# Kernel optimization log

Hardware: AMD Instinct MI355X
Metric: run time of the kernel (lower is better)

Reference implementation:

```python
import jax, jax.numpy as jnp
import numpy as np

SPACIAL_SCALE = 1.0 / 32
POOLED = 7  # original uses (pooled_height, pooled_height) for both dims


def setup_inputs() -> dict:
    key = jax.random.key(0)
    k_f, k_b, k_x, k_y = jax.random.split(key, 4)
    N, C, H, W = 4, 256, 64, 64
    R = 256
    img = 2047.0  # image-space extent (stride 32 -> 64 feature cells)
    features = jax.random.normal(k_f, (N, C, H, W), dtype=jnp.float32)
    bidx = jax.random.randint(k_b, (R,), 0, N).astype(jnp.float32)
    xs = jnp.sort(jax.random.uniform(k_x, (R, 2), dtype=jnp.float32) * img, axis=1)
    ys = jnp.sort(jax.random.uniform(k_y, (R, 2), dtype=jnp.float32) * img, axis=1)
    # roi = (batch_idx, x_min, y_min, x_max, y_max)
    rois = jnp.stack([bidx, xs[:, 0], ys[:, 0], xs[:, 1], ys[:, 1]], axis=1)
    return {"features": features, "rois": rois}


def _roi_pool(features, rois):
    N, C, H, W = features.shape
    P = POOLED
    neg = -jnp.inf

    bidx = rois[:, 0].astype(jnp.int32)
    # np.round rounds half-to-even; jnp.round matches
    bbox = jnp.round(rois[:, 1:] * SPACIAL_SCALE).astype(jnp.int32)  # [R,4]
    x0 = jnp.clip(bbox[:, 0], 0, W - 1)
    y0 = jnp.clip(bbox[:, 1], 0, H - 1)
    x1 = jnp.clip(bbox[:, 2], 0, W - 1)
    y1 = jnp.clip(bbox[:, 3], 0, H - 1)
    valid = (x0 < x1) & (y0 < y1)  # [R]

    g = features[bidx]  # [R,C,H,W] gathered per-roi feature maps
    Lh = x1 - x0  # rows (H axis) get the x-range -- quirk of the original slice
    Lw = y1 - y0  # cols (W axis) get the y-range

    idx_h = jnp.arange(H)
    idx_w = jnp.arange(W)

    # adaptive_max_pool2d bins: start=floor(i*L/P), end=ceil((i+1)*L/P)
    # Stage 1: reduce W axis into P column bins -> [R,C,H,P]
    cols = []
    for j in range(P):
        s = y0 + (j * Lw) // P
        e = y0 + ((j + 1) * Lw + P - 1) // P
        m = (idx_w[None, :] >= s[:, None]) & (idx_w[None, :] < e[:, None])  # [R,W]
        cols.append(jnp.max(jnp.where(m[:, None, None, :], g, neg), axis=-1))
    s1 = jnp.stack(cols, axis=-1)  # [R,C,H,P]

    # Stage 2: reduce H axis into P row bins -> [R,C,P,P]
    rows = []
    for i in range(P):
        s = x0 + (i * Lh) // P
        e = x0 + ((i + 1) * Lh + P - 1) // P
        m = (idx_h[None, :] >= s[:, None]) & (idx_h[None, :] < e[:, None])  # [R,H]
        rows.append(jnp.max(jnp.where(m[:, None, :, None], s1, neg), axis=2))
    out = jnp.stack(rows, axis=2)  # [R,C,P,P]

    # degenerate rois stay zero (pooled initialized with torch.zeros)
    return jnp.where(valid[:, None, None, None], out, jnp.zeros((), out.dtype))


def reference(features, rois):
    return _roi_pool(features, rois)
```

## Files before the change

kernel.cpp:

```cpp
#include <hip/hip_runtime.h>
#include <math.h>

#define P 7
#define PP (P * P)
#define C 256
#define H 64
#define W 64
#define S (H * W)
#define R_MAX 1024

#define TS 32
__global__ __launch_bounds__(256) void transpose_kernel(
    const float* __restrict__ in, float* __restrict__ outT)
{
    __shared__ float tile[TS][TS + 1];
    const int b  = blockIdx.z;
    const int s0 = blockIdx.x * TS;
    const int c0 = blockIdx.y * TS;
    const int tx = threadIdx.x;
    const int ty = threadIdx.y;

    const float* ip = in + ((size_t)b * C + c0) * S + s0;
    #pragma unroll
    for (int k = 0; k < 4; ++k)
        tile[ty + 8 * k][tx] = ip[(size_t)(ty + 8 * k) * S + tx];

    __syncthreads();

    float* op = outT + ((size_t)b * S + s0) * C + c0;
    #pragma unroll
    for (int k = 0; k < 4; ++k)
        op[(size_t)(ty + 8 * k) * C + tx] = tile[tx][ty + 8 * k];
}

__global__ __launch_bounds__(256) void bucket_kernel(
    const float* __restrict__ rois, int* __restrict__ perm, int R)
{
    __shared__ int bimg[R_MAX];
    for (int t = threadIdx.x; t < R; t += blockDim.x)
        bimg[t] = (int)rois[(size_t)t * 5];
    __syncthreads();
    for (int t = threadIdx.x; t < R; t += blockDim.x) {
        const int myb = bimg[t];
        int pos = 0;
        for (int k = 0; k < R; ++k) {
            const int bk = bimg[k];
            pos += (bk < myb) || (bk == myb && k < t);
        }
        perm[pos] = t;
    }
}

__global__ __launch_bounds__(64) void roi_pool_cell_kernel(
    const float* __restrict__ ft,
    const float* __restrict__ rois,
    const int*   __restrict__ perm,
    float* __restrict__ ws2)
{
    const int l   = blockIdx.x;
    const int nwg = gridDim.x;
    const int work = ((nwg & 7) == 0) ? ((l & 7) * (nwg >> 3) + (l >> 3)) : l;

    const int rslot = work / PP;
    const int cell  = work % PP;
    const int i     = cell / P;
    const int j     = cell % P;
    const int c4    = threadIdx.x;

    const int r = perm[rslot];

    const float* roi = rois + (size_t)r * 5;
    const int b = (int)roi[0];
    int x0 = (int)rintf(roi[1] * 0.03125f);
    int y0 = (int)rintf(roi[2] * 0.03125f);
    int x1 = (int)rintf(roi[3] * 0.03125f);
    int y1 = (int)rintf(roi[4] * 0.03125f);
    x0 = min(max(x0, 0), W - 1);
    y0 = min(max(y0, 0), H - 1);
    x1 = min(max(x1, 0), W - 1);
    y1 = min(max(y1, 0), H - 1);

    float4* o = (float4*)(ws2 + ((size_t)rslot * PP + cell) * C) + c4;

    if (!((x0 < x1) && (y0 < y1))) {
        *o = make_float4(0.0f, 0.0f, 0.0f, 0.0f);
        return;
    }

    const int Lh = x1 - x0;
    const int Lw = y1 - y0;

    const int hs = x0 + (i * Lh) / P;
    const int he = x0 + ((i + 1) * Lh + (P - 1)) / P;
    const int ws = y0 + (j * Lw) / P;
    const int we = y0 + ((j + 1) * Lw + (P - 1)) / P;

    const int bh = he - hs;
    const int bw = we - ws;

    const float* base = ft + (((size_t)b * H + hs) * W + ws) * C + c4 * 4;

    float mx = -INFINITY, my = -INFINITY, mz = -INFINITY, mw = -INFINITY;

    for (int h = 0; h < bh; h += 2) {
        const int h2 = min(h + 1, bh - 1);
        const float* r0 = base + (size_t)h  * (W * C);
        const float* r1 = base + (size_t)h2 * (W * C);
        for (int w = 0; w < bw; w += 2) {
            const int w2 = min(w + 1, bw - 1);
            const float4 a  = *(const float4*)(r0 + (size_t)w  * C);
            const float4 bb = *(const float4*)(r0 + (size_t)w2 * C);
            const float4 cc = *(const float4*)(r1 + (size_t)w  * C);
            const float4 dd = *(const float4*)(r1 + (size_t)w2 * C);
            mx = fmaxf(fmaxf(fmaxf(mx, a.x), fmaxf(bb.x, cc.x)), dd.x);
            my = fmaxf(fmaxf(fmaxf(my, a.y), fmaxf(bb.y, cc.y)), dd.y);
            mz = fmaxf(fmaxf(fmaxf(mz, a.z), fmaxf(bb.z, cc.z)), dd.z);
            mw = fmaxf(fmaxf(fmaxf(mw, a.w), fmaxf(bb.w, cc.w)), dd.w);
        }
    }

    *o = make_float4(mx, my, mz, mw);
}

#define LPAD 257
__global__ __launch_bounds__(256) void reorder_kernel(
    const float* __restrict__ ws2,
    const int*   __restrict__ perm,
    float* __restrict__ out)
{
    __shared__ float lds[PP * LPAD];
    const int l = blockIdx.x;
    const int R = gridDim.x;
    const int rslot = ((R & 7) == 0) ? ((l & 7) * (R >> 3) + (l >> 3)) : l;
    const int r = perm[rslot];
    const int tid = threadIdx.x;

    const float* src = ws2 + (size_t)rslot * PP * C;
    #pragma unroll
    for (int cell = 0; cell < PP; ++cell)
        lds[cell * LPAD + tid] = src[(size_t)cell * C + tid];

    __syncthreads();

    float* dst = out + (size_t)r * C * PP;
    const int nq = (C * PP) / 4;
    #pragma unroll
    for (int k = 0; k < 13; ++k) {
        const int q = tid + 256 * k;
        if (q < nq) {
            float v[4];
            #pragma unroll
            for (int m = 0; m < 4; ++m) {
                const int idx  = 4 * q + m;
                const int c    = idx / PP;
                const int cell = idx % PP;
                v[m] = lds[cell * LPAD + c];
            }
            *(float4*)(dst + 4 * q) = make_float4(v[0], v[1], v[2], v[3]);
        }
    }
}

__global__ __launch_bounds__(64) void roi_pool_cell_direct_kernel(
    const float* __restrict__ ft, const float* __restrict__ rois,
    float* __restrict__ out)
{
    const int bid = blockIdx.x;
    const int r   = bid / PP;
    const int rem = bid % PP;
    const int i   = rem / P;
    const int j   = rem % P;
    const int c4  = threadIdx.x;

    const float* roi = rois + (size_t)r * 5;
    const int b = (int)roi[0];
    int x0 = (int)rintf(roi[1] * 0.03125f);
    int y0 = (int)rintf(roi[2] * 0.03125f);
    int x1 = (int)rintf(roi[3] * 0.03125f);
    int y1 = (int)rintf(roi[4] * 0.03125f);
    x0 = min(max(x0, 0), W - 1);
    y0 = min(max(y0, 0), H - 1);
    x1 = min(max(x1, 0), W - 1);
    y1 = min(max(y1, 0), H - 1);

    float* o = out + (((size_t)r * C + c4 * 4) * P + i) * P + j;
    if (!((x0 < x1) && (y0 < y1))) {
        o[0] = 0.0f; o[PP] = 0.0f; o[2 * PP] = 0.0f; o[3 * PP] = 0.0f;
        return;
    }
    const int Lh = x1 - x0, Lw = y1 - y0;
    const int hs = x0 + (i * Lh) / P;
    const int he = x0 + ((i + 1) * Lh + (P - 1)) / P;
    const int ws = y0 + (j * Lw) / P;
    const int we = y0 + ((j + 1) * Lw + (P - 1)) / P;
    const int bh = he - hs, bw = we - ws;
    const float* base = ft + (((size_t)b * H + hs) * W + ws) * C + c4 * 4;
    float mx = -INFINITY, my = -INFINITY, mz = -INFINITY, mw = -INFINITY;
    for (int h = 0; h < bh; h += 2) {
        const int h2 = min(h + 1, bh - 1);
        const float* r0 = base + (size_t)h  * (W * C);
        const float* r1 = base + (size_t)h2 * (W * C);
        for (int w = 0; w < bw; w += 2) {
            const int w2 = min(w + 1, bw - 1);
            const float4 a  = *(const float4*)(r0 + (size_t)w  * C);
            const float4 bb = *(const float4*)(r0 + (size_t)w2 * C);
            const float4 cc = *(const float4*)(r1 + (size_t)w  * C);
            const float4 dd = *(const float4*)(r1 + (size_t)w2 * C);
            mx = fmaxf(fmaxf(fmaxf(mx, a.x), fmaxf(bb.x, cc.x)), dd.x);
            my = fmaxf(fmaxf(fmaxf(my, a.y), fmaxf(bb.y, cc.y)), dd.y);
            mz = fmaxf(fmaxf(fmaxf(mz, a.z), fmaxf(bb.z, cc.z)), dd.z);
            mw = fmaxf(fmaxf(fmaxf(mw, a.w), fmaxf(bb.w, cc.w)), dd.w);
        }
    }
    o[0] = mx; o[PP] = my; o[2 * PP] = mz; o[3 * PP] = mw;
}

__global__ __launch_bounds__(256) void roi_pool_naive_kernel(
    const float* __restrict__ features, const float* __restrict__ rois,
    float* __restrict__ out)
{
    const int rb = blockIdx.x;
    const int r = rb / P;
    const int i = rb % P;
    const int c = threadIdx.x;

    const float* roi = rois + (size_t)r * 5;
    const int b = (int)roi[0];
    int x0 = (int)rintf(roi[1] * 0.03125f);
    int y0 = (int)rintf(roi[2] * 0.03125f);
    int x1 = (int)rintf(roi[3] * 0.03125f);
    int y1 = (int)rintf(roi[4] * 0.03125f);
    x0 = min(max(x0, 0), W - 1);
    y0 = min(max(y0, 0), H - 1);
    x1 = min(max(x1, 0), W - 1);
    y1 = min(max(y1, 0), H - 1);

    const bool valid = (x0 < x1) && (y0 < y1);
    float* o = out + (((size_t)r * C + c) * P + i) * P;
    if (!valid) {
        #pragma unroll
        for (int j = 0; j < P; ++j) o[j] = 0.0f;
        return;
    }
    const int Lh = x1 - x0, Lw = y1 - y0;
    const int hs = x0 + (i * Lh) / P;
    const int he = x0 + ((i + 1) * Lh + (P - 1)) / P;
    int ws_[P], we_[P];
    #pragma unroll
    for (int j = 0; j < P; ++j) {
        ws_[j] = y0 + (j * Lw) / P;
        we_[j] = y0 + ((j + 1) * Lw + (P - 1)) / P;
    }
    float acc[P];
    #pragma unroll
    for (int j = 0; j < P; ++j) acc[j] = -INFINITY;
    const float* f = features + (((size_t)b * C + c) * H) * W;
    for (int h = hs; h < he; ++h) {
        const float* row = f + h * W;
        #pragma unroll
        for (int j = 0; j < P; ++j) {
            float m = acc[j];
            for (int w = ws_[j]; w < we_[j]; ++w) m = fmaxf(m, row[w]);
            acc[j] = m;
        }
    }
    #pragma unroll
    for (int j = 0; j < P; ++j) o[j] = acc[j];
}

extern "C" void kernel_launch(void* const* d_in, const int* in_sizes, int n_in,
                              void* d_out, int out_size, void* d_ws, size_t ws_size,
                              hipStream_t stream)
{
    const float* features = (const float*)d_in[0];
    const float* rois     = (const float*)d_in[1];
    float* out = (float*)d_out;

    const int R = in_sizes[1] / 5;
    const int N = in_sizes[0] / (C * S);

    const size_t ft_bytes  = (size_t)N * C * S * sizeof(float);
    const size_t ws2_bytes = (size_t)R * PP * C * sizeof(float);
    const size_t perm_bytes = (size_t)R * sizeof(int);
    const size_t full_need = ft_bytes + ws2_bytes + perm_bytes;

    if (ws_size >= full_need && R <= R_MAX) {
        float* ft  = (float*)d_ws;
        float* ws2 = (float*)((char*)d_ws + ft_bytes);
        int*  perm = (int*)((char*)d_ws + ft_bytes + ws2_bytes);

        dim3 tgrid(S / TS, C / TS, N);
        transpose_kernel<<<tgrid, dim3(TS, 8), 0, stream>>>(features, ft);
        bucket_kernel<<<1, 256, 0, stream>>>(rois, perm, R);
        roi_pool_cell_kernel<<<R * PP, 64, 0, stream>>>(ft, rois, perm, ws2);
        reorder_kernel<<<R, 256, 0, stream>>>(ws2, perm, out);
    } else if (ws_size >= ft_bytes) {
        float* ft = (float*)d_ws;
        dim3 tgrid(S / TS, C / TS, N);
        transpose_kernel<<<tgrid, dim3(TS, 8), 0, stream>>>(features, ft);
        roi_pool_cell_direct_kernel<<<R * PP, 64, 0, stream>>>(ft, rois, out);
    } else {
        roi_pool_naive_kernel<<<R * P, C, 0, stream>>>(features, rois, out);
    }
}
```

Measured before the change: 41.85 us.

## Fuse ROI pooling and output reorder into one kernel per channel group

Replaces the per-cell pooling kernel and separate reorder kernel with a single kernel where each 64-thread block handles one ROI and a 32-channel group across all 49 cells. Results are staged in shared memory and written directly in [C,P,P] order, which removes the intermediate workspace round trip and one kernel launch. Per-thread work grows to up to 7 cells with serial loops, and the work-swizzle now assumes the grid is a multiple of 8 unconditionally.

```diff
diff --git a/kernel.cpp b/kernel.cpp
--- a/kernel.cpp
+++ b/kernel.cpp
@@ -8,6 +8,11 @@
 #define W 64
 #define S (H * W)
 #define R_MAX 1024
+
+#define CH 32
+#define NCG (C / CH)
+#define ITEMS (PP * (CH / 4))
+#define LDS_PAD (PP + 1)
 
 #define TS 32
 __global__ __launch_bounds__(256) void transpose_kernel(
@@ -51,24 +56,23 @@
     }
 }
 
-__global__ __launch_bounds__(64) void roi_pool_cell_kernel(
+__global__ __launch_bounds__(64) void roi_pool_fused_kernel(
     const float* __restrict__ ft,
     const float* __restrict__ rois,
     const int*   __restrict__ perm,
-    float* __restrict__ ws2)
-{
+    float* __restrict__ out)
+{
+    __shared__ float lds[CH * LDS_PAD];
+
     const int l   = blockIdx.x;
     const int nwg = gridDim.x;
-    const int work = ((nwg & 7) == 0) ? ((l & 7) * (nwg >> 3) + (l >> 3)) : l;
-
-    const int rslot = work / PP;
-    const int cell  = work % PP;
-    const int i     = cell / P;
-    const int j     = cell % P;
-    const int c4    = threadIdx.x;
+    const int work  = (l & 7) * (nwg >> 3) + (l >> 3);
+    const int rslot = work / NCG;
+    const int cg    = work % NCG;
+    const int t     = threadIdx.x;
+    const int cbase = cg * CH;
 
     const int r = perm[rslot];
-
     const float* roi = rois + (size_t)r * 5;
     const int b = (int)roi[0];
     int x0 = (int)rintf(roi[1] * 0.03125f);
@@ -80,83 +84,84 @@
     x1 = min(max(x1, 0), W - 1);
     y1 = min(max(y1, 0), H - 1);
 
-    float4* o = (float4*)(ws2 + ((size_t)rslot * PP + cell) * C) + c4;
-
-    if (!((x0 < x1) && (y0 < y1))) {
-        *o = make_float4(0.0f, 0.0f, 0.0f, 0.0f);
-        return;
-    }
-
-    const int Lh = x1 - x0;
-    const int Lw = y1 - y0;
-
-    const int hs = x0 + (i * Lh) / P;
-    const int he = x0 + ((i + 1) * Lh + (P - 1)) / P;
-    const int ws = y0 + (j * Lw) / P;
-    const int we = y0 + ((j + 1) * Lw + (P - 1)) / P;
-
-    const int bh = he - hs;
-    const int bw = we - ws;
-
-    const float* base = ft + (((size_t)b * H + hs) * W + ws) * C + c4 * 4;
-
-    float mx = -INFINITY, my = -INFINITY, mz = -INFINITY, mw = -INFINITY;
-
-    for (int h = 0; h < bh; h += 2) {
-        const int h2 = min(h + 1, bh - 1);
-        const float* r0 = base + (size_t)h  * (W * C);
-        const float* r1 = base + (size_t)h2 * (W * C);
-        for (int w = 0; w < bw; w += 2) {
-            const int w2 = min(w + 1, bw - 1);
-            const float4 a  = *(const float4*)(r0 + (size_t)w  * C);
-            const float4 bb = *(const float4*)(r0 + (size_t)w2 * C);
-            const float4 cc = *(const float4*)(r1 + (size_t)w  * C);
-            const float4 dd = *(const float4*)(r1 + (size_t)w2 * C);
-            mx = fmaxf(fmaxf(fmaxf(mx, a.x), fmaxf(bb.x, cc.x)), dd.x);
-            my = fmaxf(fmaxf(fmaxf(my, a.y), fmaxf(bb.y, cc.y)), dd.y);
-            mz = fmaxf(fmaxf(fmaxf(mz, a.z), fmaxf(bb.z, cc.z)), dd.z);
-            mw = fmaxf(fmaxf(fmaxf(mw, a.w), fmaxf(bb.w, cc.w)), dd.w);
-        }
-    }
-
-    *o = make_float4(mx, my, mz, mw);
-}
-
-#define LPAD 257
-__global__ __launch_bounds__(256) void reorder_kernel(
-    const float* __restrict__ ws2,
-    const int*   __restrict__ perm,
-    float* __restrict__ out)
-{
-    __shared__ float lds[PP * LPAD];
-    const int l = blockIdx.x;
-    const int R = gridDim.x;
-    const int rslot = ((R & 7) == 0) ? ((l & 7) * (R >> 3) + (l >> 3)) : l;
-    const int r = perm[rslot];
-    const int tid = threadIdx.x;
-
-    const float* src = ws2 + (size_t)rslot * PP * C;
-    #pragma unroll
-    for (int cell = 0; cell < PP; ++cell)
-        lds[cell * LPAD + tid] = src[(size_t)cell * C + tid];
+    const bool valid = (x0 < x1) && (y0 < y1);
+
+    if (valid) {
+        const int Lh = x1 - x0;
+        const int Lw = y1 - y0;
+        #pragma unroll
+        for (int k = 0; k < 7; ++k) {
+            const int item = t + 64 * k;
+            if (item < ITEMS) {
+                const int cell = item >> 3;
+                const int q    = item & 7;
+                const int i    = cell / P;
+                const int j    = cell - P * i;
+
+                const int hs = x0 + (i * Lh) / P;
+                const int he = x0 + ((i + 1) * Lh + (P - 1)) / P;
+                const int ws = y0 + (j * Lw) / P;
+                const int we = y0 + ((j + 1) * Lw + (P - 1)) / P;
+                const int bh = he - hs;
+                const int bw = we - ws;
+
+                const float* base = ft + (((size_t)b * H + hs) * W + ws) * C + cbase + q * 4;
+
+                float mx = -INFINITY, my = -INFINITY, mz = -INFINITY, mw = -INFINITY;
+                for (int h = 0; h < bh; h += 2) {
+                    const int h2 = min(h + 1, bh - 1);
+                    const float* r0 = base + (size_t)h  * (W * C);
+                    const float* r1 = base + (size_t)h2 * (W * C);
+                    for (int w = 0; w < bw; w += 2) {
+                        const int w2 = min(w + 1, bw - 1);
+                        const float4 a  = *(const float4*)(r0 + (size_t)w  * C);
+                        const float4 bb = *(const float4*)(r0 + (size_t)w2 * C);
+                        const float4 cc = *(const float4*)(r1 + (size_t)w  * C);
+                        const float4 dd = *(const float4*)(r1 + (size_t)w2 * C);
+                        mx = fmaxf(fmaxf(fmaxf(mx, a.x), fmaxf(bb.x, cc.x)), dd.x);
+                        my = fmaxf(fmaxf(fmaxf(my, a.y), fmaxf(bb.y, cc.y)), dd.y);
+                        mz = fmaxf(fmaxf(fmaxf(mz, a.z), fmaxf(bb.z, cc.z)), dd.z);
+                        mw = fmaxf(fmaxf(fmaxf(mw, a.w), fmaxf(bb.w, cc.w)), dd.w);
+                    }
+                }
+                const int cl = q * 4;
+                lds[(cl + 0) * LDS_PAD + cell] = mx;
+                lds[(cl + 1) * LDS_PAD + cell] = my;
+                lds[(cl + 2) * LDS_PAD + cell] = mz;
+                lds[(cl + 3) * LDS_PAD + cell] = mw;
+            }
+        }
+    } else {
+        #pragma unroll
+        for (int k = 0; k < 7; ++k) {
+            const int item = t + 64 * k;
+            if (item < ITEMS) {
+                const int cell = item >> 3;
+                const int cl   = (item & 7) * 4;
+                lds[(cl + 0) * LDS_PAD + cell] = 0.0f;
+                lds[(cl + 1) * LDS_PAD + cell] = 0.0f;
+                lds[(cl + 2) * LDS_PAD + cell] = 0.0f;
+                lds[(cl + 3) * LDS_PAD + cell] = 0.0f;
+            }
+        }
+    }
 
     __syncthreads();
 
-    float* dst = out + (size_t)r * C * PP;
-    const int nq = (C * PP) / 4;
-    #pragma unroll
-    for (int k = 0; k < 13; ++k) {
-        const int q = tid + 256 * k;
-        if (q < nq) {
+    float* dst = out + ((size_t)r * C + cbase) * PP;
+    #pragma unroll
+    for (int k = 0; k < 7; ++k) {
+        const int fq = t + 64 * k;
+        if (fq < ITEMS) {
             float v[4];
             #pragma unroll
             for (int m = 0; m < 4; ++m) {
-                const int idx  = 4 * q + m;
-                const int c    = idx / PP;
-                const int cell = idx % PP;
-                v[m] = lds[cell * LPAD + c];
+                const int idx  = 4 * fq + m;
+                const int cl   = idx / PP;
+                const int cell = idx - PP * cl;
+                v[m] = lds[cl * LDS_PAD + cell];
             }
-            *(float4*)(dst + 4 * q) = make_float4(v[0], v[1], v[2], v[3]);
+            *(float4*)(dst + 4 * fq) = make_float4(v[0], v[1], v[2], v[3]);
         }
     }
 }
@@ -279,21 +284,18 @@
     const int R = in_sizes[1] / 5;
     const int N = in_sizes[0] / (C * S);
 
-    const size_t ft_bytes  = (size_t)N * C * S * sizeof(float);
-    const size_t ws2_bytes = (size_t)R * PP * C * sizeof(float);
+    const size_t ft_bytes   = (size_t)N * C * S * sizeof(float);
     const size_t perm_bytes = (size_t)R * sizeof(int);
-    const size_t full_need = ft_bytes + ws2_bytes + perm_bytes;
+    const size_t full_need  = ft_bytes + perm_bytes;
 
     if (ws_size >= full_need && R <= R_MAX) {
         float* ft  = (float*)d_ws;
-        float* ws2 = (float*)((char*)d_ws + ft_bytes);
-        int*  perm = (int*)((char*)d_ws + ft_bytes + ws2_bytes);
+        int*  perm = (int*)((char*)d_ws + ft_bytes);
 
         dim3 tgrid(S / TS, C / TS, N);
         transpose_kernel<<<tgrid, dim3(TS, 8), 0, stream>>>(features, ft);
         bucket_kernel<<<1, 256, 0, stream>>>(rois, perm, R);
-        roi_pool_cell_kernel<<<R * PP, 64, 0, stream>>>(ft, rois, perm, ws2);
-        reorder_kernel<<<R, 256, 0, stream>>>(ws2, perm, out);
+        roi_pool_fused_kernel<<<R * NCG, 64, 0, stream>>>(ft, rois, perm, out);
     } else if (ws_size >= ft_bytes) {
         float* ft = (float*)d_ws;
         dim3 tgrid(S / TS, C / TS, N);
```

New measurement: 65.82 us. 57.3% more time.

## Fuse bucket sort into 64x64 float4 transpose, pack two cells per pool block

Applied to the files above, without the earlier changes.

The separate bucket kernel is folded into block (0,0,0) of the transpose kernel, which saves one launch. The transpose now uses 64x64 tiles with float4 global loads and stores instead of 32x32 scalar tiles. The pooling kernel runs 128-thread blocks that each handle two output cells, which halves the number of blocks, and the last block of each ROI has an idle half-block. The risk is that block 0 of the transpose now carries the serial O(R^2) ranking work and can become a straggler, and the wider tile needs more LDS per block.

```diff
diff --git a/kernel.cpp b/kernel.cpp
--- a/kernel.cpp
+++ b/kernel.cpp
@@ -9,49 +9,62 @@
 #define S (H * W)
 #define R_MAX 1024
 
-#define TS 32
-__global__ __launch_bounds__(256) void transpose_kernel(
-    const float* __restrict__ in, float* __restrict__ outT)
-{
-    __shared__ float tile[TS][TS + 1];
-    const int b  = blockIdx.z;
-    const int s0 = blockIdx.x * TS;
-    const int c0 = blockIdx.y * TS;
-    const int tx = threadIdx.x;
-    const int ty = threadIdx.y;
-
-    const float* ip = in + ((size_t)b * C + c0) * S + s0;
-    #pragma unroll
-    for (int k = 0; k < 4; ++k)
-        tile[ty + 8 * k][tx] = ip[(size_t)(ty + 8 * k) * S + tx];
-
+#define NCP 25
+#define RPAD 257
+
+#define TT 64
+#define TPAD 65
+__global__ __launch_bounds__(256) void transpose_bucket_kernel(
+    const float* __restrict__ in, float* __restrict__ outT,
+    const float* __restrict__ rois, int* __restrict__ perm, int R)
+{
+    __shared__ float tile[TT * TPAD];
+    const int b   = blockIdx.z;
+    const int s0  = blockIdx.x * TT;
+    const int c0  = blockIdx.y * TT;
+    const int t   = threadIdx.x;
+    const int r16 = t >> 4;
+    const int m16 = (t & 15) * 4;
+
+    #pragma unroll
+    for (int k = 0; k < 4; ++k) {
+        const int cl = r16 + 16 * k;
+        const float4 v = *(const float4*)(in + (size_t)(b * C + c0 + cl) * S + s0 + m16);
+        tile[cl * TPAD + m16 + 0] = v.x;
+        tile[cl * TPAD + m16 + 1] = v.y;
+        tile[cl * TPAD + m16 + 2] = v.z;
+        tile[cl * TPAD + m16 + 3] = v.w;
+    }
     __syncthreads();
-
-    float* op = outT + ((size_t)b * S + s0) * C + c0;
-    #pragma unroll
-    for (int k = 0; k < 4; ++k)
-        op[(size_t)(ty + 8 * k) * C + tx] = tile[tx][ty + 8 * k];
-}
-
-__global__ __launch_bounds__(256) void bucket_kernel(
-    const float* __restrict__ rois, int* __restrict__ perm, int R)
-{
-    __shared__ int bimg[R_MAX];
-    for (int t = threadIdx.x; t < R; t += blockDim.x)
-        bimg[t] = (int)rois[(size_t)t * 5];
-    __syncthreads();
-    for (int t = threadIdx.x; t < R; t += blockDim.x) {
-        const int myb = bimg[t];
-        int pos = 0;
-        for (int k = 0; k < R; ++k) {
-            const int bk = bimg[k];
-            pos += (bk < myb) || (bk == myb && k < t);
-        }
-        perm[pos] = t;
-    }
-}
-
-__global__ __launch_bounds__(64) void roi_pool_cell_kernel(
+    #pragma unroll
+    for (int k = 0; k < 4; ++k) {
+        const int sl = r16 + 16 * k;
+        float4 v;
+        v.x = tile[(m16 + 0) * TPAD + sl];
+        v.y = tile[(m16 + 1) * TPAD + sl];
+        v.z = tile[(m16 + 2) * TPAD + sl];
+        v.w = tile[(m16 + 3) * TPAD + sl];
+        *(float4*)(outT + (size_t)(b * S + s0 + sl) * C + c0 + m16) = v;
+    }
+
+    if (blockIdx.x == 0 && blockIdx.y == 0 && blockIdx.z == 0 && R > 0 && R <= R_MAX) {
+        __shared__ int bimg[R_MAX];
+        for (int i = t; i < R; i += 256)
+            bimg[i] = (int)rois[(size_t)i * 5];
+        __syncthreads();
+        for (int i = t; i < R; i += 256) {
+            const int myb = bimg[i];
+            int pos = 0;
+            for (int k = 0; k < R; ++k) {
+                const int bk = bimg[k];
+                pos += (bk < myb) || (bk == myb && k < i);
+            }
+            perm[pos] = i;
+        }
+    }
+}
+
+__global__ __launch_bounds__(128) void roi_pool_cell_kernel(
     const float* __restrict__ ft,
     const float* __restrict__ rois,
     const int*   __restrict__ perm,
@@ -59,16 +72,15 @@
 {
     const int l   = blockIdx.x;
     const int nwg = gridDim.x;
-    const int work = ((nwg & 7) == 0) ? ((l & 7) * (nwg >> 3) + (l >> 3)) : l;
-
-    const int rslot = work / PP;
-    const int cell  = work % PP;
-    const int i     = cell / P;
-    const int j     = cell % P;
-    const int c4    = threadIdx.x;
+    const int work  = ((nwg & 7) == 0) ? ((l & 7) * (nwg >> 3) + (l >> 3)) : l;
+    const int rslot = work / NCP;
+    const int cp    = work % NCP;
+    const int cell  = 2 * cp + (threadIdx.x >> 6);
+    const int q     = threadIdx.x & 63;
+
+    if (cell >= PP) return;
 
     const int r = perm[rslot];
-
     const float* roi = rois + (size_t)r * 5;
     const int b = (int)roi[0];
     int x0 = (int)rintf(roi[1] * 0.03125f);
@@ -80,7 +92,7 @@
     x1 = min(max(x1, 0), W - 1);
     y1 = min(max(y1, 0), H - 1);
 
-    float4* o = (float4*)(ws2 + ((size_t)rslot * PP + cell) * C) + c4;
+    float4* o = (float4*)(ws2 + ((size_t)rslot * PP + cell) * C) + q;
 
     if (!((x0 < x1) && (y0 < y1))) {
         *o = make_float4(0.0f, 0.0f, 0.0f, 0.0f);
@@ -89,19 +101,19 @@
 
     const int Lh = x1 - x0;
     const int Lw = y1 - y0;
+    const int i  = cell / P;
+    const int j  = cell - P * i;
 
     const int hs = x0 + (i * Lh) / P;
     const int he = x0 + ((i + 1) * Lh + (P - 1)) / P;
     const int ws = y0 + (j * Lw) / P;
     const int we = y0 + ((j + 1) * Lw + (P - 1)) / P;
-
     const int bh = he - hs;
     const int bw = we - ws;
 
-    const float* base = ft + (((size_t)b * H + hs) * W + ws) * C + c4 * 4;
+    const float* base = ft + (((size_t)b * H + hs) * W + ws) * C + q * 4;
 
     float mx = -INFINITY, my = -INFINITY, mz = -INFINITY, mw = -INFINITY;
-
     for (int h = 0; h < bh; h += 2) {
         const int h2 = min(h + 1, bh - 1);
         const float* r0 = base + (size_t)h  * (W * C);
@@ -122,13 +134,12 @@
     *o = make_float4(mx, my, mz, mw);
 }
 
-#define LPAD 257
 __global__ __launch_bounds__(256) void reorder_kernel(
     const float* __restrict__ ws2,
     const int*   __restrict__ perm,
     float* __restrict__ out)
 {
-    __shared__ float lds[PP * LPAD];
+    __shared__ float lds[PP * RPAD];
     const int l = blockIdx.x;
     const int R = gridDim.x;
     const int rslot = ((R & 7) == 0) ? ((l & 7) * (R >> 3) + (l >> 3)) : l;
@@ -138,7 +149,7 @@
     const float* src = ws2 + (size_t)rslot * PP * C;
     #pragma unroll
     for (int cell = 0; cell < PP; ++cell)
-        lds[cell * LPAD + tid] = src[(size_t)cell * C + tid];
+        lds[cell * RPAD + tid] = src[(size_t)cell * C + tid];
 
     __syncthreads();
 
@@ -154,7 +165,7 @@
                 const int idx  = 4 * q + m;
                 const int c    = idx / PP;
                 const int cell = idx % PP;
-                v[m] = lds[cell * LPAD + c];
+                v[m] = lds[cell * RPAD + c];
             }
             *(float4*)(dst + 4 * q) = make_float4(v[0], v[1], v[2], v[3]);
         }
@@ -279,25 +290,24 @@
     const int R = in_sizes[1] / 5;
     const int N = in_sizes[0] / (C * S);
 
-    const size_t ft_bytes  = (size_t)N * C * S * sizeof(float);
-    const size_t ws2_bytes = (size_t)R * PP * C * sizeof(float);
+    const size_t ft_bytes   = (size_t)N * C * S * sizeof(float);
+    const size_t ws2_bytes  = (size_t)R * PP * C * sizeof(float);
     const size_t perm_bytes = (size_t)R * sizeof(int);
-    const size_t full_need = ft_bytes + ws2_bytes + perm_bytes;
+    const size_t full_need  = ft_bytes + ws2_bytes + perm_bytes;
 
     if (ws_size >= full_need && R <= R_MAX) {
         float* ft  = (float*)d_ws;
         float* ws2 = (float*)((char*)d_ws + ft_bytes);
         int*  perm = (int*)((char*)d_ws + ft_bytes + ws2_bytes);
 
-        dim3 tgrid(S / TS, C / TS, N);
-        transpose_kernel<<<tgrid, dim3(TS, 8), 0, stream>>>(features, ft);
-        bucket_kernel<<<1, 256, 0, stream>>>(rois, perm, R);
-        roi_pool_cell_kernel<<<R * PP, 64, 0, stream>>>(ft, rois, perm, ws2);
+        dim3 tgrid(S / TT, C / TT, N);
+        transpose_bucket_kernel<<<tgrid, 256, 0, stream>>>(features, ft, rois, perm, R);
+        roi_pool_cell_kernel<<<R * NCP, 128, 0, stream>>>(ft, rois, perm, ws2);
         reorder_kernel<<<R, 256, 0, stream>>>(ws2, perm, out);
     } else if (ws_size >= ft_bytes) {
         float* ft = (float*)d_ws;
-        dim3 tgrid(S / TS, C / TS, N);
-        transpose_kernel<<<tgrid, dim3(TS, 8), 0, stream>>>(features, ft);
+        dim3 tgrid(S / TT, C / TT, N);
+        transpose_bucket_kernel<<<tgrid, 256, 0, stream>>>(features, ft, rois, (int*)nullptr, 0);
         roi_pool_cell_direct_kernel<<<R * PP, 64, 0, stream>>>(ft, rois, out);
     } else {
         roi_pool_naive_kernel<<<R * P, C, 0, stream>>>(features, rois, out);
```

New measurement: 38.18 us. 1.1x faster.
